# Optimization experiments

Hardware: AMD Instinct MI355X
Metric: run time of the kernel (lower is better)

## Reference

```python
import jax, jax.numpy as jnp
import numpy as np

B, T, C, H = 4, 2048, 1024, 16
D = C // H  # head dim = 64

def setup_inputs() -> dict:
    key = jax.random.key(0)
    k1, k2, k3 = jax.random.split(key, 3)
    x = jax.random.normal(k1, (B, T, C), dtype=jnp.float32)
    w_attn = jax.random.normal(k2, (C, 3 * C), dtype=jnp.float32) * 0.02
    b_attn = jnp.zeros((3 * C,), dtype=jnp.float32)
    w_proj = jax.random.normal(k3, (C, C), dtype=jnp.float32) * 0.02
    b_proj = jnp.zeros((C,), dtype=jnp.float32)
    return {"x": x, "w_attn": w_attn, "b_attn": b_attn, "w_proj": w_proj, "b_proj": b_proj}

def reference(x, w_attn, b_attn, w_proj, b_proj):
    Bx, Tx, Cx = x.shape
    qkv = x @ w_attn + b_attn  # [B, T, 3C]
    q, k, v = jnp.split(qkv, 3, axis=2)
    # [B, H, T, D]
    q = q.reshape(Bx, Tx, H, D).swapaxes(1, 2)
    k = k.reshape(Bx, Tx, H, D).swapaxes(1, 2)
    v = v.reshape(Bx, Tx, H, D).swapaxes(1, 2)
    scale = 1.0 / jnp.sqrt(jnp.asarray(D, dtype=x.dtype))
    att = jnp.einsum('bhqd,bhkd->bhqk', q, k) * scale  # [B, H, T, T]
    causal = jnp.tril(jnp.ones((Tx, Tx), dtype=bool))
    att = jnp.where(causal[None, None], att, -jnp.inf)
    att = jax.nn.softmax(att, axis=-1)
    y = jnp.einsum('bhqk,bhkd->bhqd', att, v)  # [B, H, T, D]
    y = y.swapaxes(1, 2).reshape(Bx, Tx, Cx)
    return y @ w_proj + b_proj
```

## Files before the change

kernel.cpp:

```cpp
#include <hip/hip_runtime.h>
#include <hip/hip_bf16.h>
#include <cstdint>

#define B_ 4
#define T_ 2048
#define C_ 1024
#define H_ 16
#define D_ 64

typedef __bf16 bf16x8 __attribute__((ext_vector_type(8)));
typedef float f32x4 __attribute__((ext_vector_type(4)));

static __device__ __forceinline__ float bf2f(unsigned short u) {
    union { unsigned int i; float f; } w;
    w.i = ((unsigned int)u) << 16;
    return w.f;
}
static __device__ __forceinline__ unsigned short f2bf(float f) {
    unsigned int i = __float_as_uint(f);
    unsigned int r = (i + 0x7FFFu + ((i >> 16) & 1u)) >> 16;
    return (unsigned short)r;
}
static __device__ __forceinline__ float exp2_fast(float x) {
    float r;
    asm("v_exp_f32 %0, %1" : "=v"(r) : "v"(x));
    return r;
}

static __device__ __forceinline__ void gl_lds16(const unsigned short* g,
                                                unsigned short* l) {
    __builtin_amdgcn_global_load_lds(
        (const __attribute__((address_space(1))) unsigned int*)g,
        (__attribute__((address_space(3))) unsigned int*)l, 16, 0, 0);
}

__global__ __launch_bounds__(256)
void convert_f32_bf16(const float* __restrict__ in,
                      unsigned short* __restrict__ out, int n) {
    int i = (blockIdx.x * 256 + threadIdx.x) * 8;
    if (i < n) {
        float4 a = *(const float4*)(in + i);
        float4 b = *(const float4*)(in + i + 4);
        ushort4 s0 = {f2bf(a.x), f2bf(a.y), f2bf(a.z), f2bf(a.w)};
        ushort4 s1 = {f2bf(b.x), f2bf(b.y), f2bf(b.z), f2bf(b.w)};
        *(ushort4*)(out + i) = s0;
        *(ushort4*)(out + i + 4) = s1;
    }
}

__global__ void transpose_f32_bf16(const float* __restrict__ in,
                                   unsigned short* __restrict__ out,
                                   int R, int Cc) {
    __shared__ unsigned short tile[32][33];
    int c0 = blockIdx.x * 32;
    int r0 = blockIdx.y * 32;
    int tx = threadIdx.x, ty = threadIdx.y;
    #pragma unroll
    for (int i = ty; i < 32; i += 8)
        tile[i][tx] = f2bf(in[(size_t)(r0 + i) * Cc + c0 + tx]);
    __syncthreads();
    #pragma unroll
    for (int i = ty; i < 32; i += 8)
        out[(size_t)(c0 + i) * R + r0 + tx] = tile[tx][i];
}

__global__ __launch_bounds__(256)
void gemm_qkv(const unsigned short* __restrict__ A,
              const unsigned short* __restrict__ Bt,
              const float* __restrict__ bias,
              unsigned short* __restrict__ qkv,
              unsigned short* __restrict__ vt,
              int M, float qscale) {
    const int N = 3 * C_, K = C_;
    __shared__ __align__(16) unsigned short As[128][32];
    __shared__ __align__(16) unsigned short Bs[128][32];

    int tid = threadIdx.x;
    int row0 = blockIdx.y * 128;
    int col0 = blockIdx.x * 128;
    int wave = tid >> 6;
    int lane = tid & 63;
    int wm = wave >> 1, wn = wave & 1;
    int m16 = lane & 15, quad = lane >> 4;

    f32x4 acc[4][4];
    #pragma unroll
    for (int i = 0; i < 4; ++i)
        #pragma unroll
        for (int j = 0; j < 4; ++j)
            acc[i][j] = (f32x4){0.f, 0.f, 0.f, 0.f};

    for (int k0 = 0; k0 < K; k0 += 32) {
        #pragma unroll
        for (int it = 0; it < 2; ++it) {
            int c = tid + it * 256;
            int r = c >> 2, ko = (c & 3) << 3;
            gl_lds16(A + (size_t)(row0 + r) * K + k0 + ko, &As[0][0] + (size_t)c * 8);
            gl_lds16(Bt + (size_t)(col0 + r) * K + k0 + ko, &Bs[0][0] + (size_t)c * 8);
        }
        __syncthreads();

        bf16x8 af[4], bfr[4];
        #pragma unroll
        for (int i = 0; i < 4; ++i)
            af[i] = *(const bf16x8*)&As[wm * 64 + i * 16 + m16][quad * 8];
        #pragma unroll
        for (int j = 0; j < 4; ++j)
            bfr[j] = *(const bf16x8*)&Bs[wn * 64 + j * 16 + m16][quad * 8];
        #pragma unroll
        for (int i = 0; i < 4; ++i)
            #pragma unroll
            for (int j = 0; j < 4; ++j)
                acc[i][j] = __builtin_amdgcn_mfma_f32_16x16x32_bf16(
                    af[i], bfr[j], acc[i][j], 0, 0, 0);
        __syncthreads();
    }

    float bv[4];
    #pragma unroll
    for (int j = 0; j < 4; ++j)
        bv[j] = bias[col0 + wn * 64 + j * 16 + m16];

    unsigned short* wbuf = &As[0][0] + wave * 2048;
    bool isV = (col0 >= 2 * C_);
    float sc = (col0 < C_) ? qscale : 1.0f;
    int b_loc = row0 >> 11;
    int trow0 = (row0 & 2047) + wm * 64;

    #pragma unroll
    for (int sub = 0; sub < 4; ++sub) {
        int i0 = (sub >> 1) << 1;
        int j0 = (sub & 1) << 1;
        #pragma unroll
        for (int jj = 0; jj < 2; ++jj) {
            #pragma unroll
            for (int ii = 0; ii < 2; ++ii) {
                #pragma unroll
                for (int rr = 0; rr < 4; ++rr) {
                    int rl = ii * 16 + quad * 4 + rr;
                    int cl = jj * 16 + m16;
                    unsigned short hv =
                        f2bf((acc[i0 + ii][j0 + jj][rr] + bv[j0 + jj]) * sc);
                    if (!isV) wbuf[rl * 40 + cl] = hv;
                    else      wbuf[cl * 40 + rl] = hv;
                }
            }
        }
        __builtin_amdgcn_sched_barrier(0);
        if (!isV) {
            #pragma unroll
            for (int it = 0; it < 4; ++it) {
                int rl = it * 8 + (lane >> 3);
                int cc = (lane & 7) << 2;
                uint2 v2 = *(const uint2*)&wbuf[rl * 40 + cc];
                int rowg = row0 + wm * 64 + i0 * 16 + rl;
                int colg = col0 + wn * 64 + j0 * 16 + cc;
                *(uint2*)&qkv[(size_t)rowg * (2 * C_) + colg] = v2;
            }
        } else {
            int head = ((col0 - 2 * C_) + wn * 64) >> 6;
            unsigned short* vtb =
                vt + (size_t)((b_loc * H_ + head) * 64) * T_;
            #pragma unroll
            for (int it = 0; it < 4; ++it) {
                int dsub = it * 8 + (lane >> 3);
                int tc = (lane & 7) << 2;
                uint2 v2 = *(const uint2*)&wbuf[dsub * 40 + tc];
                int d = j0 * 16 + dsub;
                int tg = trow0 + i0 * 16 + tc;
                *(uint2*)&vtb[(size_t)d * T_ + tg] = v2;
            }
        }
        __builtin_amdgcn_sched_barrier(0);
    }
}

__global__ __launch_bounds__(256)
void gemm_out(const unsigned short* __restrict__ A, int lda,
              const unsigned short* __restrict__ Bt,
              const float* __restrict__ bias,
              float* __restrict__ Cmat,
              int M, int N, int K) {
    __shared__ __align__(16) unsigned short As[128][32];
    __shared__ __align__(16) unsigned short Bs[128][32];

    int tid = threadIdx.x;
    int row0 = blockIdx.y * 128;
    int col0 = blockIdx.x * 128;
    int wave = tid >> 6;
    int lane = tid & 63;
    int wm = wave >> 1, wn = wave & 1;
    int m16 = lane & 15, quad = lane >> 4;

    f32x4 acc[4][4];
    #pragma unroll
    for (int i = 0; i < 4; ++i)
        #pragma unroll
        for (int j = 0; j < 4; ++j)
            acc[i][j] = (f32x4){0.f, 0.f, 0.f, 0.f};

    for (int k0 = 0; k0 < K; k0 += 32) {
        #pragma unroll
        for (int it = 0; it < 2; ++it) {
            int c = tid + it * 256;
            int r = c >> 2, ko = (c & 3) << 3;
            gl_lds16(A + (size_t)(row0 + r) * lda + k0 + ko, &As[0][0] + (size_t)c * 8);
            gl_lds16(Bt + (size_t)(col0 + r) * K + k0 + ko, &Bs[0][0] + (size_t)c * 8);
        }
        __syncthreads();

        bf16x8 af[4], bfr[4];
        #pragma unroll
        for (int i = 0; i < 4; ++i)
            af[i] = *(const bf16x8*)&As[wm * 64 + i * 16 + m16][quad * 8];
        #pragma unroll
        for (int j = 0; j < 4; ++j)
            bfr[j] = *(const bf16x8*)&Bs[wn * 64 + j * 16 + m16][quad * 8];
        #pragma unroll
        for (int i = 0; i < 4; ++i)
            #pragma unroll
            for (int j = 0; j < 4; ++j)
                acc[i][j] = __builtin_amdgcn_mfma_f32_16x16x32_bf16(
                    af[i], bfr[j], acc[i][j], 0, 0, 0);
        __syncthreads();
    }

    #pragma unroll
    for (int j = 0; j < 4; ++j) {
        int col = col0 + wn * 64 + j * 16 + m16;
        float bvv = bias[col];
        #pragma unroll
        for (int i = 0; i < 4; ++i) {
            int row = row0 + wm * 64 + i * 16 + quad * 4;
            #pragma unroll
            for (int rr = 0; rr < 4; ++rr)
                Cmat[(size_t)(row + rr) * N + col] = acc[i][j][rr] + bvv;
        }
    }
}

__global__ __launch_bounds__(256)
void attn_mfma(unsigned short* __restrict__ qkv,
               const unsigned short* __restrict__ vt) {
    __shared__ __align__(16) unsigned short Ks[2][64][80];
    __shared__ __align__(16) unsigned short Vs[2][64][80];
    __shared__ __align__(16) unsigned short Pb[4][16][72];

    int bh = blockIdx.x;
    int b = bh >> 4, h = bh & 15;
    int qb = (T_ / 64 - 1) - blockIdx.y;
    int tid = threadIdx.x;
    int wave = tid >> 6;
    int lane = tid & 63;
    int m16 = lane & 15, quad = lane >> 4;

    const size_t rs = 2 * C_;
    unsigned short* base = qkv + (size_t)b * T_ * rs + h * 64;
    const unsigned short* kb0 = base + C_;
    const unsigned short* vtb = vt + (size_t)bh * 64 * T_;

    int qrow = qb * 64 + wave * 16 + m16;
    const unsigned short* qp = base + (size_t)qrow * rs;
    bf16x8 qf0 = *(const bf16x8*)(qp + quad * 8);
    bf16x8 qf1 = *(const bf16x8*)(qp + 32 + quad * 8);

    f32x4 o[4];
    #pragma unroll
    for (int dt = 0; dt < 4; ++dt) o[dt] = (f32x4){0.f, 0.f, 0.f, 0.f};
    float lrow[4] = {0.f, 0.f, 0.f, 0.f};

    int qg0 = qb * 64 + wave * 16 + quad * 4;
    int ntiles = qb + 1;

    int kkey = tid >> 3, kdc = (tid & 7) << 3;
    int vd   = tid >> 3, vkc = (tid & 7) << 3;

    uint4 ra  = *(const uint4*)(kb0 + (size_t)kkey * rs + kdc);
    uint4 rb  = *(const uint4*)(kb0 + (size_t)(kkey + 32) * rs + kdc);
    uint4 rva = *(const uint4*)(vtb + (size_t)vd * T_ + vkc);
    uint4 rvb = *(const uint4*)(vtb + (size_t)(vd + 32) * T_ + vkc);
    *(uint4*)&Ks[0][kkey][kdc]      = ra;
    *(uint4*)&Ks[0][kkey + 32][kdc] = rb;
    *(uint4*)&Vs[0][vd][vkc]        = rva;
    *(uint4*)&Vs[0][vd + 32][vkc]   = rvb;
    if (ntiles > 1) {
        const unsigned short* kn = kb0 + (size_t)64 * rs;
        ra  = *(const uint4*)(kn + (size_t)kkey * rs + kdc);
        rb  = *(const uint4*)(kn + (size_t)(kkey + 32) * rs + kdc);
        rva = *(const uint4*)(vtb + (size_t)vd * T_ + 64 + vkc);
        rvb = *(const uint4*)(vtb + (size_t)(vd + 32) * T_ + 64 + vkc);
    }
    __syncthreads();

    for (int kt = 0; kt < ntiles; ++kt) {
        int cur = kt & 1;

        f32x4 s[4];
        #pragma unroll
        for (int st = 0; st < 4; ++st) {
            f32x4 acc = (f32x4){0.f, 0.f, 0.f, 0.f};
            bf16x8 k0 = *(const bf16x8*)&Ks[cur][st * 16 + m16][quad * 8];
            bf16x8 k1 = *(const bf16x8*)&Ks[cur][st * 16 + m16][32 + quad * 8];
            acc = __builtin_amdgcn_mfma_f32_16x16x32_bf16(qf0, k0, acc, 0, 0, 0);
            acc = __builtin_amdgcn_mfma_f32_16x16x32_bf16(qf1, k1, acc, 0, 0, 0);
            s[st] = acc;
        }

        if (kt == qb) {
            #pragma unroll
            for (int st = 0; st < 4; ++st) {
                int kg = kt * 64 + st * 16 + m16;
                #pragma unroll
                for (int r = 0; r < 4; ++r)
                    if (kg > qg0 + r) s[st][r] = -1.0e30f;
            }
        }

        #pragma unroll
        for (int st = 0; st < 4; ++st) {
            #pragma unroll
            for (int r = 0; r < 4; ++r) {
                float p = exp2_fast(s[st][r]);
                lrow[r] += p;
                Pb[wave][quad * 4 + r][st * 16 + m16] = f2bf(p);
            }
        }
        __builtin_amdgcn_sched_barrier(0);

        #pragma unroll
        for (int s2 = 0; s2 < 2; ++s2) {
            bf16x8 pa = *(const bf16x8*)&Pb[wave][m16][s2 * 32 + quad * 8];
            #pragma unroll
            for (int dt = 0; dt < 4; ++dt) {
                bf16x8 vv = *(const bf16x8*)&Vs[cur][dt * 16 + m16][s2 * 32 + quad * 8];
                o[dt] = __builtin_amdgcn_mfma_f32_16x16x32_bf16(pa, vv, o[dt], 0, 0, 0);
            }
        }

        if (kt + 1 < ntiles) {
            int nxt = (kt + 1) & 1;
            *(uint4*)&Ks[nxt][kkey][kdc]      = ra;
            *(uint4*)&Ks[nxt][kkey + 32][kdc] = rb;
            *(uint4*)&Vs[nxt][vd][vkc]        = rva;
            *(uint4*)&Vs[nxt][vd + 32][vkc]   = rvb;
            if (kt + 2 < ntiles) {
                const unsigned short* kn = kb0 + (size_t)((kt + 2) * 64) * rs;
                ra  = *(const uint4*)(kn + (size_t)kkey * rs + kdc);
                rb  = *(const uint4*)(kn + (size_t)(kkey + 32) * rs + kdc);
                rva = *(const uint4*)(vtb + (size_t)vd * T_ + (kt + 2) * 64 + vkc);
                rvb = *(const uint4*)(vtb + (size_t)(vd + 32) * T_ + (kt + 2) * 64 + vkc);
            }
        }
        __syncthreads();
    }

    float lf[4];
    #pragma unroll
    for (int r = 0; r < 4; ++r) lf[r] = lrow[r];
    #pragma unroll
    for (int off = 1; off <= 8; off <<= 1)
        #pragma unroll
        for (int r = 0; r < 4; ++r)
            lf[r] += __shfl_xor(lf[r], off);

    #pragma unroll
    for (int r = 0; r < 4; ++r) {
        float inv = 1.0f / lf[r];
        unsigned short* op = base + (size_t)(qg0 + r) * rs;
        #pragma unroll
        for (int dt = 0; dt < 4; ++dt)
            op[dt * 16 + m16] = f2bf(o[dt][r] * inv);
    }
}

extern "C" void kernel_launch(void* const* d_in, const int* in_sizes, int n_in,
                              void* d_out, int out_size, void* d_ws, size_t ws_size,
                              hipStream_t stream) {
    const float* x      = (const float*)d_in[0];
    const float* w_attn = (const float*)d_in[1];
    const float* b_attn = (const float*)d_in[2];
    const float* w_proj = (const float*)d_in[3];
    const float* b_proj = (const float*)d_in[4];
    float* out = (float*)d_out;

    unsigned short* ws = (unsigned short*)d_ws;
    unsigned short* xb       = ws;
    unsigned short* w_attn_t = xb + (size_t)B_ * T_ * C_;
    unsigned short* w_proj_t = w_attn_t + (size_t)3 * C_ * C_;
    unsigned short* qkv      = w_proj_t + (size_t)C_ * C_;

    const size_t fixed_hw = (size_t)B_ * T_ * C_ + 4 * (size_t)C_ * C_;
    const size_t per_b_hw = (size_t)T_ * 2 * C_ + (size_t)H_ * 64 * T_;
    int bstep = (ws_size >= (fixed_hw + (size_t)B_ * per_b_hw) * sizeof(unsigned short))
                ? B_ : 1;

    int nx = B_ * T_ * C_;
    convert_f32_bf16<<<nx / 2048, 256, 0, stream>>>(x, xb, nx);
    transpose_f32_bf16<<<dim3(3 * C_ / 32, C_ / 32), dim3(32, 8), 0, stream>>>(
        w_attn, w_attn_t, C_, 3 * C_);
    transpose_f32_bf16<<<dim3(C_ / 32, C_ / 32), dim3(32, 8), 0, stream>>>(
        w_proj, w_proj_t, C_, C_);

    const float QSCALE = 0.125f * 1.44269504088896341f;

    for (int b0 = 0; b0 < B_; b0 += bstep) {
        int M = bstep * T_;
        const unsigned short* xbb = xb + (size_t)b0 * T_ * C_;
        float* ob = out + (size_t)b0 * T_ * C_;
        unsigned short* vt = qkv + (size_t)bstep * T_ * 2 * C_;

        gemm_qkv<<<dim3(3 * C_ / 128, M / 128), 256, 0, stream>>>(
            xbb, w_attn_t, b_attn, qkv, vt, M, QSCALE);

        attn_mfma<<<dim3(bstep * H_, T_ / 64), 256, 0, stream>>>(qkv, vt);

        gemm_out<<<dim3(C_ / 128, M / 128), 256, 0, stream>>>(
            qkv, 2 * C_, w_proj_t, b_proj, ob, M, C_, C_);
    }
}
```

Baseline: 263.4 us.

## Double-buffer GEMM k-loop with BK=64, XOR-swizzled LDS, and tile swizzle

```diff
diff --git a/kernel.cpp b/kernel.cpp
--- a/kernel.cpp
+++ b/kernel.cpp
@@ -8,14 +8,14 @@
 #define H_ 16
 #define D_ 64
 
+#define BM 128
+#define BN 128
+#define BK 64
+#define NT (C_ / BK)
+
 typedef __bf16 bf16x8 __attribute__((ext_vector_type(8)));
 typedef float f32x4 __attribute__((ext_vector_type(4)));
 
-static __device__ __forceinline__ float bf2f(unsigned short u) {
-    union { unsigned int i; float f; } w;
-    w.i = ((unsigned int)u) << 16;
-    return w.f;
-}
 static __device__ __forceinline__ unsigned short f2bf(float f) {
     unsigned int i = __float_as_uint(f);
     unsigned int r = (i + 0x7FFFu + ((i >> 16) & 1u)) >> 16;
@@ -64,68 +64,100 @@
         out[(size_t)(c0 + i) * R + r0 + tx] = tile[tx][i];
 }
 
-__global__ __launch_bounds__(256)
+#define GEMM128_CORE(APTR, ASTRIDE, BTPTR)                                    \
+    int tid = threadIdx.x;                                                    \
+    int nwg = gridDim.x * gridDim.y;                                          \
+    int flat = blockIdx.y * gridDim.x + blockIdx.x;                           \
+    int swz = (flat & 7) * (nwg >> 3) + (flat >> 3);                          \
+    int bx = swz % gridDim.x;                                                 \
+    int by = swz / gridDim.x;                                                 \
+    int row0 = by * BM;                                                       \
+    int col0 = bx * BN;                                                       \
+    int wave = tid >> 6, lane = tid & 63;                                     \
+    int wm = wave >> 1, wn = wave & 1;                                        \
+    int m16 = lane & 15, quad = lane >> 4;                                    \
+    int srow = tid >> 3;                                                      \
+    int scs = ((tid & 7) ^ (srow & 7)) * 8;                                   \
+    const unsigned short* aps = (APTR) + (size_t)(row0 + srow) * (ASTRIDE)    \
+                                + scs;                                        \
+    const unsigned short* bps = (BTPTR) + (size_t)(col0 + srow) * C_ + scs;   \
+    f32x4 acc[4][4];                                                          \
+    _Pragma("unroll")                                                         \
+    for (int i = 0; i < 4; ++i)                                               \
+    _Pragma("unroll")                                                         \
+    for (int j = 0; j < 4; ++j)                                               \
+        acc[i][j] = (f32x4){0.f, 0.f, 0.f, 0.f};                              \
+    auto STAGE = [&](int t, int buf) {                                        \
+        int koff = t * BK;                                                    \
+        unsigned short* ad = smem + buf * 8192 + tid * 8;                     \
+        unsigned short* bd = smem + 16384 + buf * 8192 + tid * 8;             \
+        _Pragma("unroll")                                                     \
+        for (int l = 0; l < 4; ++l) {                                         \
+            gl_lds16(aps + (size_t)(l * 32) * (ASTRIDE) + koff, ad + l * 2048);\
+            gl_lds16(bps + (size_t)(l * 32) * C_ + koff, bd + l * 2048);      \
+        }                                                                     \
+    };                                                                        \
+    int rbA = wm * 64 + m16;                                                  \
+    int rbB = wn * 64 + m16;                                                  \
+    int pc0 = ((0 + quad) ^ (m16 & 7)) * 8;                                   \
+    int pc1 = ((4 + quad) ^ (m16 & 7)) * 8;                                   \
+    STAGE(0, 0);                                                              \
+    asm volatile("s_waitcnt vmcnt(0)" ::: "memory");                          \
+    __builtin_amdgcn_s_barrier();                                             \
+    for (int t = 0; t < NT; ++t) {                                            \
+        int buf = t & 1;                                                      \
+        if (t + 1 < NT) STAGE(t + 1, buf ^ 1);                                \
+        const unsigned short* Abuf = smem + buf * 8192;                       \
+        const unsigned short* Bbuf = smem + 16384 + buf * 8192;               \
+        bf16x8 a0[4], a1[4], b0[4], b1[4];                                    \
+        _Pragma("unroll")                                                     \
+        for (int i = 0; i < 4; ++i) {                                         \
+            a0[i] = *(const bf16x8*)(Abuf + (rbA + i * 16) * 64 + pc0);       \
+            a1[i] = *(const bf16x8*)(Abuf + (rbA + i * 16) * 64 + pc1);       \
+        }                                                                     \
+        _Pragma("unroll")                                                     \
+        for (int j = 0; j < 4; ++j) {                                         \
+            b0[j] = *(const bf16x8*)(Bbuf + (rbB + j * 16) * 64 + pc0);       \
+            b1[j] = *(const bf16x8*)(Bbuf + (rbB + j * 16) * 64 + pc1);       \
+        }                                                                     \
+        __builtin_amdgcn_s_setprio(1);                                        \
+        _Pragma("unroll")                                                     \
+        for (int i = 0; i < 4; ++i)                                           \
+        _Pragma("unroll")                                                     \
+        for (int j = 0; j < 4; ++j) {                                         \
+            acc[i][j] = __builtin_amdgcn_mfma_f32_16x16x32_bf16(              \
+                a0[i], b0[j], acc[i][j], 0, 0, 0);                            \
+            acc[i][j] = __builtin_amdgcn_mfma_f32_16x16x32_bf16(              \
+                a1[i], b1[j], acc[i][j], 0, 0, 0);                            \
+        }                                                                     \
+        __builtin_amdgcn_s_setprio(0);                                        \
+        asm volatile("s_waitcnt vmcnt(0)" ::: "memory");                      \
+        __builtin_amdgcn_s_barrier();                                        \
+    }                                                                         \
+    __syncthreads();
+
+__global__ __launch_bounds__(256, 2)
 void gemm_qkv(const unsigned short* __restrict__ A,
               const unsigned short* __restrict__ Bt,
               const float* __restrict__ bias,
               unsigned short* __restrict__ qkv,
               unsigned short* __restrict__ vt,
               int M, float qscale) {
-    const int N = 3 * C_, K = C_;
-    __shared__ __align__(16) unsigned short As[128][32];
-    __shared__ __align__(16) unsigned short Bs[128][32];
-
-    int tid = threadIdx.x;
-    int row0 = blockIdx.y * 128;
-    int col0 = blockIdx.x * 128;
-    int wave = tid >> 6;
-    int lane = tid & 63;
-    int wm = wave >> 1, wn = wave & 1;
-    int m16 = lane & 15, quad = lane >> 4;
-
-    f32x4 acc[4][4];
-    #pragma unroll
-    for (int i = 0; i < 4; ++i)
-        #pragma unroll
-        for (int j = 0; j < 4; ++j)
-            acc[i][j] = (f32x4){0.f, 0.f, 0.f, 0.f};
-
-    for (int k0 = 0; k0 < K; k0 += 32) {
-        #pragma unroll
-        for (int it = 0; it < 2; ++it) {
-            int c = tid + it * 256;
-            int r = c >> 2, ko = (c & 3) << 3;
-            gl_lds16(A + (size_t)(row0 + r) * K + k0 + ko, &As[0][0] + (size_t)c * 8);
-            gl_lds16(Bt + (size_t)(col0 + r) * K + k0 + ko, &Bs[0][0] + (size_t)c * 8);
-        }
-        __syncthreads();
-
-        bf16x8 af[4], bfr[4];
-        #pragma unroll
-        for (int i = 0; i < 4; ++i)
-            af[i] = *(const bf16x8*)&As[wm * 64 + i * 16 + m16][quad * 8];
-        #pragma unroll
-        for (int j = 0; j < 4; ++j)
-            bfr[j] = *(const bf16x8*)&Bs[wn * 64 + j * 16 + m16][quad * 8];
-        #pragma unroll
-        for (int i = 0; i < 4; ++i)
-            #pragma unroll
-            for (int j = 0; j < 4; ++j)
-                acc[i][j] = __builtin_amdgcn_mfma_f32_16x16x32_bf16(
-                    af[i], bfr[j], acc[i][j], 0, 0, 0);
-        __syncthreads();
-    }
+    __shared__ __align__(16) unsigned short smem[32768];
+    GEMM128_CORE(A, C_, Bt)
 
     float bv[4];
     #pragma unroll
     for (int j = 0; j < 4; ++j)
         bv[j] = bias[col0 + wn * 64 + j * 16 + m16];
 
-    unsigned short* wbuf = &As[0][0] + wave * 2048;
+    unsigned short* wbuf = smem + wave * 2048;
     bool isV = (col0 >= 2 * C_);
     float sc = (col0 < C_) ? qscale : 1.0f;
     int b_loc = row0 >> 11;
     int trow0 = (row0 & 2047) + wm * 64;
+    int head = isV ? ((col0 - 2 * C_ + wn * 64) >> 6) : 0;
+    unsigned short* vtb = vt + (size_t)((b_loc * H_ + head) * 64) * T_;
 
     #pragma unroll
     for (int sub = 0; sub < 4; ++sub) {
@@ -158,9 +190,6 @@
                 *(uint2*)&qkv[(size_t)rowg * (2 * C_) + colg] = v2;
             }
         } else {
-            int head = ((col0 - 2 * C_) + wn * 64) >> 6;
-            unsigned short* vtb =
-                vt + (size_t)((b_loc * H_ + head) * 64) * T_;
             #pragma unroll
             for (int it = 0; it < 4; ++it) {
                 int dsub = it * 8 + (lane >> 3);
@@ -175,55 +204,15 @@
     }
 }
 
-__global__ __launch_bounds__(256)
-void gemm_out(const unsigned short* __restrict__ A, int lda,
+__global__ __launch_bounds__(256, 2)
+void gemm_out(const unsigned short* __restrict__ A,
               const unsigned short* __restrict__ Bt,
               const float* __restrict__ bias,
               float* __restrict__ Cmat,
-              int M, int N, int K) {
-    __shared__ __align__(16) unsigned short As[128][32];
-    __shared__ __align__(16) unsigned short Bs[128][32];
-
-    int tid = threadIdx.x;
-    int row0 = blockIdx.y * 128;
-    int col0 = blockIdx.x * 128;
-    int wave = tid >> 6;
-    int lane = tid & 63;
-    int wm = wave >> 1, wn = wave & 1;
-    int m16 = lane & 15, quad = lane >> 4;
-
-    f32x4 acc[4][4];
-    #pragma unroll
-    for (int i = 0; i < 4; ++i)
-        #pragma unroll
-        for (int j = 0; j < 4; ++j)
-            acc[i][j] = (f32x4){0.f, 0.f, 0.f, 0.f};
-
-    for (int k0 = 0; k0 < K; k0 += 32) {
-        #pragma unroll
-        for (int it = 0; it < 2; ++it) {
-            int c = tid + it * 256;
-            int r = c >> 2, ko = (c & 3) << 3;
-            gl_lds16(A + (size_t)(row0 + r) * lda + k0 + ko, &As[0][0] + (size_t)c * 8);
-            gl_lds16(Bt + (size_t)(col0 + r) * K + k0 + ko, &Bs[0][0] + (size_t)c * 8);
-        }
-        __syncthreads();
-
-        bf16x8 af[4], bfr[4];
-        #pragma unroll
-        for (int i = 0; i < 4; ++i)
-            af[i] = *(const bf16x8*)&As[wm * 64 + i * 16 + m16][quad * 8];
-        #pragma unroll
-        for (int j = 0; j < 4; ++j)
-            bfr[j] = *(const bf16x8*)&Bs[wn * 64 + j * 16 + m16][quad * 8];
-        #pragma unroll
-        for (int i = 0; i < 4; ++i)
-            #pragma unroll
-            for (int j = 0; j < 4; ++j)
-                acc[i][j] = __builtin_amdgcn_mfma_f32_16x16x32_bf16(
-                    af[i], bfr[j], acc[i][j], 0, 0, 0);
-        __syncthreads();
-    }
+              int M) {
+    const int N = C_;
+    __shared__ __align__(16) unsigned short smem[32768];
+    GEMM128_CORE(A, (2 * C_), Bt)
 
     #pragma unroll
     for (int j = 0; j < 4; ++j) {
@@ -242,8 +231,8 @@
 __global__ __launch_bounds__(256)
 void attn_mfma(unsigned short* __restrict__ qkv,
                const unsigned short* __restrict__ vt) {
-    __shared__ __align__(16) unsigned short Ks[2][64][80];
-    __shared__ __align__(16) unsigned short Vs[2][64][80];
+    __shared__ __align__(16) unsigned short Ks[2][64][64];
+    __shared__ __align__(16) unsigned short Vs[2][64][64];
     __shared__ __align__(16) unsigned short Pb[4][16][72];
 
     int bh = blockIdx.x;
@@ -273,22 +262,26 @@
     int ntiles = qb + 1;
 
     int kkey = tid >> 3, kdc = (tid & 7) << 3;
-    int vd   = tid >> 3, vkc = (tid & 7) << 3;
+    int kswz = (((tid & 7) ^ (kkey & 7)) << 3);
+    int vd = kkey, vswz = kswz;
+
+    int kpc0 = ((0 + quad) ^ (m16 & 7)) << 3;
+    int kpc1 = ((4 + quad) ^ (m16 & 7)) << 3;
 
     uint4 ra  = *(const uint4*)(kb0 + (size_t)kkey * rs + kdc);
     uint4 rb  = *(const uint4*)(kb0 + (size_t)(kkey + 32) * rs + kdc);
-    uint4 rva = *(const uint4*)(vtb + (size_t)vd * T_ + vkc);
-    uint4 rvb = *(const uint4*)(vtb + (size_t)(vd + 32) * T_ + vkc);
-    *(uint4*)&Ks[0][kkey][kdc]      = ra;
-    *(uint4*)&Ks[0][kkey + 32][kdc] = rb;
-    *(uint4*)&Vs[0][vd][vkc]        = rva;
-    *(uint4*)&Vs[0][vd + 32][vkc]   = rvb;
+    uint4 rva = *(const uint4*)(vtb + (size_t)vd * T_ + kdc);
+    uint4 rvb = *(const uint4*)(vtb + (size_t)(vd + 32) * T_ + kdc);
+    *(uint4*)&Ks[0][kkey][kswz]      = ra;
+    *(uint4*)&Ks[0][kkey + 32][kswz] = rb;
+    *(uint4*)&Vs[0][vd][vswz]        = rva;
+    *(uint4*)&Vs[0][vd + 32][vswz]   = rvb;
     if (ntiles > 1) {
         const unsigned short* kn = kb0 + (size_t)64 * rs;
         ra  = *(const uint4*)(kn + (size_t)kkey * rs + kdc);
         rb  = *(const uint4*)(kn + (size_t)(kkey + 32) * rs + kdc);
-        rva = *(const uint4*)(vtb + (size_t)vd * T_ + 64 + vkc);
-        rvb = *(const uint4*)(vtb + (size_t)(vd + 32) * T_ + 64 + vkc);
+        rva = *(const uint4*)(vtb + (size_t)vd * T_ + 64 + kdc);
+        rvb = *(const uint4*)(vtb + (size_t)(vd + 32) * T_ + 64 + kdc);
     }
     __syncthreads();
 
@@ -299,8 +292,8 @@
         #pragma unroll
         for (int st = 0; st < 4; ++st) {
             f32x4 acc = (f32x4){0.f, 0.f, 0.f, 0.f};
-            bf16x8 k0 = *(const bf16x8*)&Ks[cur][st * 16 + m16][quad * 8];
-            bf16x8 k1 = *(const bf16x8*)&Ks[cur][st * 16 + m16][32 + quad * 8];
+            bf16x8 k0 = *(const bf16x8*)&Ks[cur][st * 16 + m16][kpc0];
+            bf16x8 k1 = *(const bf16x8*)&Ks[cur][st * 16 + m16][kpc1];
             acc = __builtin_amdgcn_mfma_f32_16x16x32_bf16(qf0, k0, acc, 0, 0, 0);
             acc = __builtin_amdgcn_mfma_f32_16x16x32_bf16(qf1, k1, acc, 0, 0, 0);
             s[st] = acc;
@@ -330,25 +323,26 @@
         #pragma unroll
         for (int s2 = 0; s2 < 2; ++s2) {
             bf16x8 pa = *(const bf16x8*)&Pb[wave][m16][s2 * 32 + quad * 8];
+            int vpc = ((s2 * 4 + quad) ^ (m16 & 7)) << 3;
             #pragma unroll
             for (int dt = 0; dt < 4; ++dt) {
-                bf16x8 vv = *(const bf16x8*)&Vs[cur][dt * 16 + m16][s2 * 32 + quad * 8];
+                bf16x8 vv = *(const bf16x8*)&Vs[cur][dt * 16 + m16][vpc];
                 o[dt] = __builtin_amdgcn_mfma_f32_16x16x32_bf16(pa, vv, o[dt], 0, 0, 0);
             }
         }
 
         if (kt + 1 < ntiles) {
             int nxt = (kt + 1) & 1;
-            *(uint4*)&Ks[nxt][kkey][kdc]      = ra;
-            *(uint4*)&Ks[nxt][kkey + 32][kdc] = rb;
-            *(uint4*)&Vs[nxt][vd][vkc]        = rva;
-            *(uint4*)&Vs[nxt][vd + 32][vkc]   = rvb;
+            *(uint4*)&Ks[nxt][kkey][kswz]      = ra;
+            *(uint4*)&Ks[nxt][kkey + 32][kswz] = rb;
+            *(uint4*)&Vs[nxt][vd][vswz]        = rva;
+            *(uint4*)&Vs[nxt][vd + 32][vswz]   = rvb;
             if (kt + 2 < ntiles) {
                 const unsigned short* kn = kb0 + (size_t)((kt + 2) * 64) * rs;
                 ra  = *(const uint4*)(kn + (size_t)kkey * rs + kdc);
                 rb  = *(const uint4*)(kn + (size_t)(kkey + 32) * rs + kdc);
-                rva = *(const uint4*)(vtb + (size_t)vd * T_ + (kt + 2) * 64 + vkc);
-                rvb = *(const uint4*)(vtb + (size_t)(vd + 32) * T_ + (kt + 2) * 64 + vkc);
+                rva = *(const uint4*)(vtb + (size_t)vd * T_ + (kt + 2) * 64 + kdc);
+                rvb = *(const uint4*)(vtb + (size_t)(vd + 32) * T_ + (kt + 2) * 64 + kdc);
             }
         }
         __syncthreads();
@@ -406,15 +400,14 @@
     for (int b0 = 0; b0 < B_; b0 += bstep) {
         int M = bstep * T_;
         const unsigned short* xbb = xb + (size_t)b0 * T_ * C_;
-        float* ob = out + (size_t)b0 * T_ * C_;
         unsigned short* vt = qkv + (size_t)bstep * T_ * 2 * C_;
 
-        gemm_qkv<<<dim3(3 * C_ / 128, M / 128), 256, 0, stream>>>(
+        gemm_qkv<<<dim3(3 * C_ / BN, M / BM), 256, 0, stream>>>(
             xbb, w_attn_t, b_attn, qkv, vt, M, QSCALE);
 
         attn_mfma<<<dim3(bstep * H_, T_ / 64), 256, 0, stream>>>(qkv, vt);
 
-        gemm_out<<<dim3(C_ / 128, M / 128), 256, 0, stream>>>(
-            qkv, 2 * C_, w_proj_t, b_proj, ob, M, C_, C_);
-    }
-}
+        gemm_out<<<dim3(C_ / BN, M / BM), 256, 0, stream>>>(
+            qkv, w_proj_t, b_proj, out + (size_t)b0 * T_ * C_, M);
+    }
+}
```

Measured after the change: 258.1 us. -2.0%, faster.
